# Kernel tuning notes

Hardware: AMD Instinct MI355X
Metric: run time of the kernel (lower is better)

## Reference

```python
import jax, jax.numpy as jnp
from jax import lax
import numpy as np

B, C, H, W = 32, 3, 512, 512


def _erode3(m):
    # cv2.erode with 3x3 ones kernel == 3x3 min-pool; cv2's default border value
    # for erode is +inf, which matches reduce_window's min identity under SAME padding.
    return lax.reduce_window(m, jnp.inf, lax.min, (1, 3, 3), (1, 1, 1), 'SAME')


def _dilate3(m):
    # cv2.dilate with 3x3 ones kernel == 3x3 max-pool; default border -inf matches max identity.
    return lax.reduce_window(m, -jnp.inf, lax.max, (1, 3, 3), (1, 1, 1), 'SAME')


def setup_inputs() -> dict:
    key = jax.random.key(0)
    k1, k2 = jax.random.split(key)
    yhat = jax.random.normal(k1, (B, C, H, W), dtype=jnp.float32)
    y = jax.random.randint(k2, (B, H, W), 0, 3, dtype=jnp.int32)
    return {"yhat": yhat, "y": y}


def reference(yhat, y):
    # softmax + argmax over class dim (argmax(softmax(x)) == argmax(x), kept faithful)
    probas = jnp.argmax(jax.nn.softmax(yhat, axis=1), axis=1).astype(jnp.int32)  # [B,H,W]

    m1 = (y == 1).astype(jnp.float32)
    m2 = (y == 2).astype(jnp.float32)

    e1 = _erode3(m1)
    d1 = _dilate3(m1)
    e2 = _erode3(m2)
    d2 = _dilate3(m2)

    # class 2 assignment overrides class 1 (matches sequential masked assignment order)
    eroded = jnp.where(e2 == 1, 2, jnp.where(e1 == 1, 1, 0)).astype(jnp.int32)
    dilated = jnp.where(d2 == 1, 2, jnp.where(d1 == 1, 1, 0)).astype(jnp.int32)

    inter = jnp.logical_and(dilated == probas, dilated != 0)
    inter_count = jnp.sum(inter, axis=(1, 2))  # [B]
    uni = jnp.logical_or(eroded != 0, probas != 0)
    uni_count = jnp.sum(uni, axis=(1, 2))  # [B]

    score = inter_count.astype(jnp.float32) / uni_count.astype(jnp.float32)
    return jnp.mean(score)
```

## Files before the change

### kernel.cpp

```cpp
#include <hip/hip_runtime.h>

#define IMG_H 512
#define IMG_W 512
#define NB    32
#define HW    (IMG_H * IMG_W)
#define SEGS  32
#define NPART 256

__device__ __forceinline__ unsigned build16(const int* __restrict__ row) {
    unsigned m = 0u;
    #pragma unroll
    for (int q = 0; q < 4; ++q) {
        const int4 w = *reinterpret_cast<const int4*>(row + 4 * q);
        m |= ((w.x == 1) ? 1u : 0u) << (4 * q + 0);
        m |= ((w.y == 1) ? 1u : 0u) << (4 * q + 1);
        m |= ((w.z == 1) ? 1u : 0u) << (4 * q + 2);
        m |= ((w.w == 1) ? 1u : 0u) << (4 * q + 3);
        m |= ((w.x == 2) ? 1u : 0u) << (16 + 4 * q + 0);
        m |= ((w.y == 2) ? 1u : 0u) << (16 + 4 * q + 1);
        m |= ((w.z == 2) ? 1u : 0u) << (16 + 4 * q + 2);
        m |= ((w.w == 2) ? 1u : 0u) << (16 + 4 * q + 3);
    }
    return m;
}

__global__ __launch_bounds__(64) void iou_kernel(const float* __restrict__ yhat,
                                                 const int* __restrict__ y,
                                                 unsigned long long* __restrict__ part) {
    const int b    = blockIdx.y;
    const int lane = threadIdx.x;
    const int t    = blockIdx.x * 64 + lane;
    const int h    = t >> 5;
    const int seg  = t & 31;
    const int wbase = seg << 4;
    const bool lowHalf = (lane < 32);

    const int* yb = y + (size_t)b * HW;
    const int ho  = lowHalf ? (h - 1) : (h + 1);
    const bool ov = (unsigned)ho < IMG_H;
    const int hoc = ov ? ho : h;

    const unsigned mOwn = build16(yb + (size_t)h   * IMG_W + wbase);
    const unsigned mOut = build16(yb + (size_t)hoc * IMG_W + wbase);

    const float* yh = yhat + (size_t)b * 3 * HW + (size_t)h * IMG_W + wbase;
    const float4 qa0 = *reinterpret_cast<const float4*>(yh);
    const float4 qa1 = *reinterpret_cast<const float4*>(yh + 4);
    const float4 qa2 = *reinterpret_cast<const float4*>(yh + 8);
    const float4 qa3 = *reinterpret_cast<const float4*>(yh + 12);
    const float4 qb0 = *reinterpret_cast<const float4*>(yh + HW);
    const float4 qb1 = *reinterpret_cast<const float4*>(yh + HW + 4);
    const float4 qb2 = *reinterpret_cast<const float4*>(yh + HW + 8);
    const float4 qb3 = *reinterpret_cast<const float4*>(yh + HW + 12);
    const float4 qc0 = *reinterpret_cast<const float4*>(yh + 2 * HW);
    const float4 qc1 = *reinterpret_cast<const float4*>(yh + 2 * HW + 4);
    const float4 qc2 = *reinterpret_cast<const float4*>(yh + 2 * HW + 8);
    const float4 qc3 = *reinterpret_cast<const float4*>(yh + 2 * HW + 12);

    const unsigned mPar = __shfl(mOwn, lane ^ 32, 64);
    const unsigned mT = lowHalf ? mOut : mPar;
    const unsigned mB = lowHalf ? mPar : mOut;
    const bool vT = lowHalf ? ov : true;
    const bool vB = lowHalf ? true : ov;

    const int laneL = (lane + 63) & 63;
    const int laneR = (lane + 1) & 63;
    const unsigned tL = __shfl(mT, laneL, 64),   tR = __shfl(mT, laneR, 64);
    const unsigned cL = __shfl(mOwn, laneL, 64), cR = __shfl(mOwn, laneR, 64);
    const unsigned bL = __shfl(mB, laneL, 64),   bR = __shfl(mB, laneR, 64);

    #define EXT1(m, ml, mr) ((((m) & 0xFFFFu) << 1) | (((ml) >> 15) & 1u) | (((mr) & 1u) << 17))
    #define EXT2(m, ml, mr) ((((m) >> 16) << 1)     | ((ml) >> 31)        | ((((mr) >> 16) & 1u) << 17))
    const unsigned eT1 = EXT1(mT, tL, tR),   eT2 = EXT2(mT, tL, tR);
    const unsigned eC1 = EXT1(mOwn, cL, cR), eC2 = EXT2(mOwn, cL, cR);
    const unsigned eB1 = EXT1(mB, bL, bR),   eB2 = EXT2(mB, bL, bR);

    const unsigned ALL = 0x3FFFFu;
    unsigned vmask = ALL;
    if (seg == 0)        vmask &= ~1u;
    if (seg == SEGS - 1) vmask &= ~(1u << 17);
    const unsigned inv = ALL & ~vmask;

    unsigned and1 = eC1 & (vT ? eT1 : ALL) & (vB ? eB1 : ALL);
    unsigned and2 = eC2 & (vT ? eT2 : ALL) & (vB ? eB2 : ALL);
    unsigned or1  = eC1 | (vT ? eT1 : 0u)  | (vB ? eB1 : 0u);
    unsigned or2  = eC2 | (vT ? eT2 : 0u)  | (vB ? eB2 : 0u);
    and1 |= inv;   and2 |= inv;
    or1  &= vmask; or2  &= vmask;

    const unsigned E1 = and1 & (and1 >> 1) & (and1 >> 2);
    const unsigned E2 = and2 & (and2 >> 1) & (and2 >> 2);
    const unsigned D1 = or1  | (or1  >> 1) | (or1  >> 2);
    const unsigned D2 = or2  | (or2  >> 1) | (or2  >> 2);

    const float A[16]  = {qa0.x,qa0.y,qa0.z,qa0.w, qa1.x,qa1.y,qa1.z,qa1.w,
                          qa2.x,qa2.y,qa2.z,qa2.w, qa3.x,qa3.y,qa3.z,qa3.w};
    const float Bv[16] = {qb0.x,qb0.y,qb0.z,qb0.w, qb1.x,qb1.y,qb1.z,qb1.w,
                          qb2.x,qb2.y,qb2.z,qb2.w, qb3.x,qb3.y,qb3.z,qb3.w};
    const float Cv[16] = {qc0.x,qc0.y,qc0.z,qc0.w, qc1.x,qc1.y,qc1.z,qc1.w,
                          qc2.x,qc2.y,qc2.z,qc2.w, qc3.x,qc3.y,qc3.z,qc3.w};
    unsigned P1 = 0u, P2 = 0u;
    #pragma unroll
    for (int j = 0; j < 16; ++j) {
        int   p    = 0;
        float best = A[j];
        if (Bv[j] > best) { best = Bv[j]; p = 1; }
        if (Cv[j] > best) {               p = 2; }
        P1 |= ((p == 1) ? 1u : 0u) << j;
        P2 |= ((p == 2) ? 1u : 0u) << j;
    }

    const unsigned inter = (unsigned)__popc((D2 & P2) | (D1 & ~D2 & P1));
    const unsigned uni   = (unsigned)__popc((E1 | E2 | P1 | P2) & 0xFFFFu);

    unsigned long long packed = (unsigned long long)inter | ((unsigned long long)uni << 32);
    #pragma unroll
    for (int off = 32; off > 0; off >>= 1)
        packed += __shfl_down(packed, off, 64);
    if (lane == 0)
        part[(size_t)b * NPART + blockIdx.x] = packed;
}

__global__ void finalize_kernel(const unsigned long long* __restrict__ part,
                                float* __restrict__ out) {
    const int t = threadIdx.x;
    const int b = t >> 3;
    const int k = t & 7;
    unsigned long long s = 0ull;
    #pragma unroll
    for (int i = 0; i < 32; ++i)
        s += part[(size_t)b * NPART + k * 32 + i];
    s += __shfl_down(s, 4, 8);
    s += __shfl_down(s, 2, 8);
    s += __shfl_down(s, 1, 8);

    __shared__ float r[NB];
    if (k == 0) {
        const float inter = (float)(unsigned int)(s & 0xFFFFFFFFull);
        const float uni   = (float)(unsigned int)(s >> 32);
        r[b] = inter / uni;
    }
    __syncthreads();
    if (t < 32) {
        float v = r[t];
        #pragma unroll
        for (int off = 16; off > 0; off >>= 1)
            v += __shfl_down(v, off, 32);
        if (t == 0) out[0] = v / (float)NB;
    }
}

extern "C" void kernel_launch(void* const* d_in, const int* in_sizes, int n_in,
                              void* d_out, int out_size, void* d_ws, size_t ws_size,
                              hipStream_t stream) {
    const float* yhat = (const float*)d_in[0];
    const int*   y    = (const int*)d_in[1];
    float*       out  = (float*)d_out;
    unsigned long long* part = (unsigned long long*)d_ws;

    dim3 grid(NPART, NB, 1);
    iou_kernel<<<grid, 64, 0, stream>>>(yhat, y, part);
    finalize_kernel<<<1, 256, 0, stream>>>(part, out);
}
```

Baseline: 34.06 us.

## Fuse finalize into main kernel via last-block atomic counter, larger blocks

```diff
diff --git a/kernel.cpp b/kernel.cpp
--- a/kernel.cpp
+++ b/kernel.cpp
@@ -5,34 +5,37 @@
 #define NB    32
 #define HW    (IMG_H * IMG_W)
 #define SEGS  32
-#define NPART 256
+#define RPB   8
+#define GX    (IMG_H / RPB)
+#define NPART GX
+#define NBLK  (GX * NB)
 
 __device__ __forceinline__ unsigned build16(const int* __restrict__ row) {
     unsigned m = 0u;
     #pragma unroll
     for (int q = 0; q < 4; ++q) {
         const int4 w = *reinterpret_cast<const int4*>(row + 4 * q);
-        m |= ((w.x == 1) ? 1u : 0u) << (4 * q + 0);
-        m |= ((w.y == 1) ? 1u : 0u) << (4 * q + 1);
-        m |= ((w.z == 1) ? 1u : 0u) << (4 * q + 2);
-        m |= ((w.w == 1) ? 1u : 0u) << (4 * q + 3);
-        m |= ((w.x == 2) ? 1u : 0u) << (16 + 4 * q + 0);
-        m |= ((w.y == 2) ? 1u : 0u) << (16 + 4 * q + 1);
-        m |= ((w.z == 2) ? 1u : 0u) << (16 + 4 * q + 2);
-        m |= ((w.w == 2) ? 1u : 0u) << (16 + 4 * q + 3);
+        const unsigned b1 = (unsigned)(w.x & 1)        | ((unsigned)(w.y & 1) << 1)
+                          | ((unsigned)(w.z & 1) << 2) | ((unsigned)(w.w & 1) << 3);
+        const unsigned b2 = (unsigned)(w.x >> 1)        | ((unsigned)(w.y >> 1) << 1)
+                          | ((unsigned)(w.z >> 1) << 2) | ((unsigned)(w.w >> 1) << 3);
+        m |= (b1 << (4 * q)) | (b2 << (16 + 4 * q));
     }
     return m;
 }
 
-__global__ __launch_bounds__(64) void iou_kernel(const float* __restrict__ yhat,
-                                                 const int* __restrict__ y,
-                                                 unsigned long long* __restrict__ part) {
-    const int b    = blockIdx.y;
-    const int lane = threadIdx.x;
-    const int t    = blockIdx.x * 64 + lane;
-    const int h    = t >> 5;
-    const int seg  = t & 31;
+__global__ __launch_bounds__(256) void iou_kernel(const float* __restrict__ yhat,
+                                                  const int* __restrict__ y,
+                                                  unsigned long long* __restrict__ part,
+                                                  unsigned long long* __restrict__ ctr,
+                                                  float* __restrict__ out) {
+    const int b   = blockIdx.y;
+    const int t   = blockIdx.x * 256 + threadIdx.x;
+    const int h   = t >> 5;
+    const int seg = t & 31;
     const int wbase = seg << 4;
+
+    const int lane     = threadIdx.x & 63;
     const bool lowHalf = (lane < 32);
 
     const int* yb = y + (size_t)b * HW;
@@ -102,12 +105,11 @@
     unsigned P1 = 0u, P2 = 0u;
     #pragma unroll
     for (int j = 0; j < 16; ++j) {
-        int   p    = 0;
-        float best = A[j];
-        if (Bv[j] > best) { best = Bv[j]; p = 1; }
-        if (Cv[j] > best) {               p = 2; }
-        P1 |= ((p == 1) ? 1u : 0u) << j;
-        P2 |= ((p == 2) ? 1u : 0u) << j;
+        const bool bgt = Bv[j] > A[j];
+        const bool c2  = Cv[j] > fmaxf(A[j], Bv[j]);
+        const bool c1  = bgt && !c2;
+        P1 |= (c1 ? 1u : 0u) << j;
+        P2 |= (c2 ? 1u : 0u) << j;
     }
 
     const unsigned inter = (unsigned)__popc((D2 & P2) | (D1 & ~D2 & P1));
@@ -117,36 +119,47 @@
     #pragma unroll
     for (int off = 32; off > 0; off >>= 1)
         packed += __shfl_down(packed, off, 64);
-    if (lane == 0)
-        part[(size_t)b * NPART + blockIdx.x] = packed;
-}
 
-__global__ void finalize_kernel(const unsigned long long* __restrict__ part,
-                                float* __restrict__ out) {
-    const int t = threadIdx.x;
-    const int b = t >> 3;
-    const int k = t & 7;
-    unsigned long long s = 0ull;
-    #pragma unroll
-    for (int i = 0; i < 32; ++i)
-        s += part[(size_t)b * NPART + k * 32 + i];
-    s += __shfl_down(s, 4, 8);
-    s += __shfl_down(s, 2, 8);
-    s += __shfl_down(s, 1, 8);
-
-    __shared__ float r[NB];
-    if (k == 0) {
-        const float inter = (float)(unsigned int)(s & 0xFFFFFFFFull);
-        const float uni   = (float)(unsigned int)(s >> 32);
-        r[b] = inter / uni;
+    __shared__ unsigned long long wsum[4];
+    __shared__ int amLast;
+    const int wave = threadIdx.x >> 6;
+    if ((threadIdx.x & 63) == 0) wsum[wave] = packed;
+    __syncthreads();
+    if (threadIdx.x == 0) {
+        part[(size_t)b * NPART + blockIdx.x] = wsum[0] + wsum[1] + wsum[2] + wsum[3];
+        __threadfence();
+        const unsigned long long old = atomicAdd(ctr, 1ull);
+        amLast = (old == (unsigned long long)(NBLK - 1)) ? 1 : 0;
     }
     __syncthreads();
-    if (t < 32) {
-        float v = r[t];
+
+    if (amLast) {
+        __threadfence();
+        const int tt = threadIdx.x;
+        const int bb = tt >> 3;
+        const int k  = tt & 7;
+        unsigned long long s = 0ull;
         #pragma unroll
-        for (int off = 16; off > 0; off >>= 1)
-            v += __shfl_down(v, off, 32);
-        if (t == 0) out[0] = v / (float)NB;
+        for (int i = 0; i < 8; ++i)
+            s += part[(size_t)bb * NPART + k * 8 + i];
+        s += __shfl_down(s, 4, 8);
+        s += __shfl_down(s, 2, 8);
+        s += __shfl_down(s, 1, 8);
+
+        __shared__ float r[NB];
+        if (k == 0) {
+            const float fi = (float)(unsigned int)(s & 0xFFFFFFFFull);
+            const float fu = (float)(unsigned int)(s >> 32);
+            r[bb] = fi / fu;
+        }
+        __syncthreads();
+        if (tt < 32) {
+            float v = r[tt];
+            #pragma unroll
+            for (int off = 16; off > 0; off >>= 1)
+                v += __shfl_down(v, off, 32);
+            if (tt == 0) out[0] = v / (float)NB;
+        }
     }
 }
 
@@ -156,9 +169,11 @@
     const float* yhat = (const float*)d_in[0];
     const int*   y    = (const int*)d_in[1];
     float*       out  = (float*)d_out;
-    unsigned long long* part = (unsigned long long*)d_ws;
+    unsigned long long* ctr  = (unsigned long long*)d_ws;
+    unsigned long long* part = (unsigned long long*)d_ws + 16;
 
-    dim3 grid(NPART, NB, 1);
-    iou_kernel<<<grid, 64, 0, stream>>>(yhat, y, part);
-    finalize_kernel<<<1, 256, 0, stream>>>(part, out);
+    hipMemsetAsync(d_ws, 0, sizeof(unsigned long long), stream);
+
+    dim3 grid(GX, NB, 1);
+    iou_kernel<<<grid, 256, 0, stream>>>(yhat, y, part, ctr, out);
 }
```

Measured after the change: 94.00 us. 176% more time.
